# Optimization experiments

Hardware: AMD Instinct MI355X
Metric: run time of the kernel (lower is better)

## Reference

```python
import jax, jax.numpy as jnp
import numpy as np

# Mamba2 dims (from source: d_model=2048, d_state=64, d_conv=4, expand=2; defaults headdim=64, ngroups=1)
D_MODEL = 2048
D_STATE = 64
D_CONV = 4
EXPAND = 2
HEADDIM = 64
D_INNER = EXPAND * D_MODEL            # 4096
NHEADS = D_INNER // HEADDIM           # 64
NGROUPS = 1
CONV_DIM = D_INNER + 2 * NGROUPS * D_STATE   # 4224
D_IN_PROJ = 2 * D_INNER + 2 * NGROUPS * D_STATE + NHEADS  # 8384
N_CLASSES = 4
EPS = 1e-5


def setup_inputs() -> dict:
    key = jax.random.key(0)
    ks = jax.random.split(key, 10)
    b, l = 4, 2048
    x = jax.random.normal(ks[0], (b, l, D_MODEL), dtype=jnp.float32)
    in_proj_w = jax.random.normal(ks[1], (D_IN_PROJ, D_MODEL), dtype=jnp.float32) * 0.02
    conv_w = jax.random.normal(ks[2], (CONV_DIM, D_CONV), dtype=jnp.float32) * 0.2
    conv_b = jnp.zeros((CONV_DIM,), dtype=jnp.float32)
    # dt_bias s.t. softplus(dt_bias) in [0.001, 0.1]
    dt = jax.random.uniform(ks[3], (NHEADS,), minval=0.001, maxval=0.1)
    dt_bias = jnp.log(jnp.expm1(dt)).astype(jnp.float32)
    # A in [1, 16] per head
    A_log = jnp.log(jax.random.uniform(ks[4], (NHEADS,), minval=1.0, maxval=16.0)).astype(jnp.float32)
    D = jnp.ones((NHEADS,), dtype=jnp.float32)
    norm_w = jnp.ones((D_INNER,), dtype=jnp.float32)
    out_proj_w = jax.random.normal(ks[5], (D_MODEL, D_INNER), dtype=jnp.float32) * 0.02
    cls_w = jax.random.normal(ks[6], (N_CLASSES, D_MODEL), dtype=jnp.float32) * 0.02
    cls_b = jnp.zeros((N_CLASSES,), dtype=jnp.float32)
    return {"x": x, "in_proj_w": in_proj_w, "conv_w": conv_w, "conv_b": conv_b,
            "dt_bias": dt_bias, "A_log": A_log, "D": D, "norm_w": norm_w,
            "out_proj_w": out_proj_w, "cls_w": cls_w, "cls_b": cls_b}


def _mamba2_forward(x, in_proj_w, conv_w, conv_b, dt_bias, A_log, D, norm_w, out_proj_w):
    b, l, _ = x.shape
    zxbcdt = jnp.einsum('bld,ed->ble', x, in_proj_w)  # (b,l,8384)
    z = zxbcdt[..., :D_INNER]
    xBC = zxbcdt[..., D_INNER:D_INNER + CONV_DIM]
    dt_raw = zxbcdt[..., D_INNER + CONV_DIM:]         # (b,l,nheads)

    # causal depthwise conv1d (kernel D_CONV), then SiLU
    xp = jnp.pad(xBC, ((0, 0), (D_CONV - 1, 0), (0, 0)))
    conv_out = conv_b
    for k in range(D_CONV):
        conv_out = conv_out + xp[:, k:k + l, :] * conv_w[:, k]
    xBC = jax.nn.silu(conv_out)

    xh = xBC[..., :D_INNER].reshape(b, l, NHEADS, HEADDIM)
    Bm = xBC[..., D_INNER:D_INNER + D_STATE]          # (b,l,n) ngroups=1
    Cm = xBC[..., D_INNER + D_STATE:]                 # (b,l,n)

    dt = jax.nn.softplus(dt_raw + dt_bias)           # (b,l,h)
    dA = jnp.exp(dt * (-jnp.exp(A_log)))             # (b,l,h)
    dtx = dt[..., None] * xh                          # (b,l,h,p)

    xs = (dA.transpose(1, 0, 2), dtx.transpose(1, 0, 2, 3),
          Bm.transpose(1, 0, 2), Cm.transpose(1, 0, 2))

    def step(hst, inp):
        dA_t, dtx_t, B_t, C_t = inp
        # hst: (b,h,p,n)
        hst = hst * dA_t[:, :, None, None] + dtx_t[..., None] * B_t[:, None, None, :]
        y_t = jnp.einsum('bhpn,bn->bhp', hst, C_t)
        return hst, y_t

    h0 = jnp.zeros((b, NHEADS, HEADDIM, D_STATE), dtype=x.dtype)
    _, ys = jax.lax.scan(step, h0, xs)               # (l,b,h,p)
    y = ys.transpose(1, 0, 2, 3) + D[None, None, :, None] * xh
    y = y.reshape(b, l, D_INNER)

    # RMSNormGated (norm_before_gate=False): rmsnorm(y * silu(z)) * weight
    y = y * jax.nn.silu(z)
    y = y * jax.lax.rsqrt(jnp.mean(y * y, axis=-1, keepdims=True) + EPS) * norm_w
    return jnp.einsum('ble,de->bld', y, out_proj_w)   # (b,l,d_model)


def reference(x, in_proj_w, conv_w, conv_b, dt_bias, A_log, D, norm_w, out_proj_w, cls_w, cls_b):
    h = _mamba2_forward(x, in_proj_w, conv_w, conv_b, dt_bias, A_log, D, norm_w, out_proj_w)
    return jnp.einsum('bld,cd->blc', h, cls_w) + cls_b  # (b,l,4)
```

## Files before the change

kernel.cpp:

```cpp
#include <hip/hip_runtime.h>

#define BB 4
#define LL 2048
#define DMODEL 2048
#define DSTATE 64
#define DCONV 4
#define DINNER 4096
#define NHEADS 64
#define CONVDIM 4224
#define DINPROJ 8384
#define NPAD1   8448
#define MROWS 8192
#define DTROW0 8320
#define XBCCOLS 4288

typedef short bf16x8 __attribute__((ext_vector_type(8)));
typedef float f32x4  __attribute__((ext_vector_type(4)));
typedef __attribute__((address_space(1))) void as1_void;
typedef __attribute__((address_space(3))) void as3_void;

__device__ inline unsigned short f2bf(float f) {
  unsigned int u = __float_as_uint(f);
  u += 0x7FFF + ((u >> 16) & 1);
  return (unsigned short)(u >> 16);
}
__device__ inline float bf2f(unsigned short u) {
  return __uint_as_float(((unsigned int)u) << 16);
}

__global__ void f32_to_bf16_kernel(const float* __restrict__ in,
                                   unsigned short* __restrict__ out, long nquads) {
  long q = (long)blockIdx.x * 256 + threadIdx.x;
  if (q >= nquads) return;
  float4 v = ((const float4*)in)[q];
  ushort4 o;
  o.x = f2bf(v.x); o.y = f2bf(v.y); o.z = f2bf(v.z); o.w = f2bf(v.w);
  ((ushort4*)out)[q] = o;
}

__global__ void convert_w1_kernel(const float* __restrict__ w,
                                  unsigned short* __restrict__ out) {
  long q = (long)blockIdx.x * 256 + threadIdx.x;
  long row = q >> 9;
  ushort4 o; o.x = 0; o.y = 0; o.z = 0; o.w = 0;
  if (row < DINPROJ) {
    float4 v = ((const float4*)w)[q];
    o.x = f2bf(v.x); o.y = f2bf(v.y); o.z = f2bf(v.z); o.w = f2bf(v.w);
  }
  ((ushort4*)out)[q] = o;
}

template <bool BF16OUT, bool SPLIT>
__global__ __launch_bounds__(256) void gemm_mfma(
    const unsigned short* __restrict__ A,
    const unsigned short* __restrict__ B,
    void* __restrict__ Cv, void* __restrict__ Cv2,
    int M, int N, int K, int Nsplit, int ld2) {
  __shared__ __align__(16) char sA[128 * 128];
  __shared__ __align__(16) char sB[128 * 128];
  const int tid  = threadIdx.x;
  const int lane = tid & 63;
  const int wave = tid >> 6;
  const long m0 = (long)blockIdx.y * 128;
  const long n0 = (long)blockIdx.x * 128;
  const int wm = (wave >> 1) * 64;
  const int wn = (wave & 1) * 64;
  const int fr = lane & 15;
  const int kb = lane >> 4;
  const int xr = (fr & 7) << 4;
  const size_t strideA = (size_t)K * 2;

  f32x4 acc[4][4] = {};

  for (int k0 = 0; k0 < K; k0 += 64) {
    __syncthreads();
#pragma unroll
    for (int u = 0; u < 4; ++u) {
      const int idx  = u * 256 + tid;
      const int row  = idx >> 3;
      const int csrc = ((idx & 7) << 4) ^ ((row & 7) << 4);
      const char* ga = (const char*)A + (size_t)(m0 + row) * strideA + (size_t)k0 * 2 + csrc;
      const char* gb = (const char*)B + (size_t)(n0 + row) * strideA + (size_t)k0 * 2 + csrc;
      __builtin_amdgcn_global_load_lds((as1_void*)ga, (as3_void*)(sA + idx * 16), 16, 0, 0);
      __builtin_amdgcn_global_load_lds((as1_void*)gb, (as3_void*)(sB + idx * 16), 16, 0, 0);
    }
    __syncthreads();
#pragma unroll
    for (int kh = 0; kh < 2; ++kh) {
      bf16x8 af[4], bg[4];
      const int cread = (kh * 64 + kb * 16) ^ xr;
#pragma unroll
      for (int i = 0; i < 4; ++i) {
        const int ar = wm + i * 16 + fr;
        af[i] = *(const bf16x8*)(sA + ar * 128 + cread);
        const int br = wn + i * 16 + fr;
        bg[i] = *(const bf16x8*)(sB + br * 128 + cread);
      }
#pragma unroll
      for (int i = 0; i < 4; ++i)
#pragma unroll
        for (int j = 0; j < 4; ++j)
          acc[i][j] = __builtin_amdgcn_mfma_f32_16x16x32_bf16(af[i], bg[j], acc[i][j], 0, 0, 0);
    }
  }

#pragma unroll
  for (int i = 0; i < 4; ++i) {
    const long mbase = m0 + wm + i * 16 + kb * 4;
#pragma unroll
    for (int j = 0; j < 4; ++j) {
      const long n = n0 + wn + j * 16 + fr;
      if (n < N) {
#pragma unroll
        for (int r = 0; r < 4; ++r) {
          const long m = mbase + r;
          if (!SPLIT || n < Nsplit) {
            const long ld = SPLIT ? Nsplit : N;
            if (BF16OUT) ((unsigned short*)Cv)[m * ld + n] = f2bf(acc[i][j][r]);
            else         ((float*)Cv)[m * ld + n] = acc[i][j][r];
          } else {
            if (BF16OUT) ((unsigned short*)Cv2)[m * (long)ld2 + (n - Nsplit)] = f2bf(acc[i][j][r]);
            else         ((float*)Cv2)[m * (long)ld2 + (n - Nsplit)] = acc[i][j][r];
          }
        }
      }
    }
  }
}

__global__ void dt_kernel(const float* __restrict__ x,
                          const float* __restrict__ w,
                          const float* __restrict__ dt_bias,
                          const float* __restrict__ A_log,
                          float* __restrict__ dtv, float* __restrict__ dAv) {
  __shared__ float s_w[64][129];
  __shared__ float s_x[16][129];
  const int tid = threadIdx.x;
  const int row0 = blockIdx.x * 16;
  const int c = tid & 63;
  const int rg = tid >> 6;
  float acc[4] = {0.f, 0.f, 0.f, 0.f};
  for (int k0 = 0; k0 < DMODEL; k0 += 128) {
    __syncthreads();
#pragma unroll
    for (int u = 0; u < 32; ++u) {
      int idx = u * 256 + tid;
      int r = idx >> 7, kk = idx & 127;
      s_w[r][kk] = w[(size_t)(DTROW0 + r) * DMODEL + k0 + kk];
    }
#pragma unroll
    for (int u = 0; u < 8; ++u) {
      int idx = u * 256 + tid;
      int r = idx >> 7, kk = idx & 127;
      s_x[r][kk] = x[(size_t)(row0 + r) * DMODEL + k0 + kk];
    }
    __syncthreads();
    for (int kk = 0; kk < 128; ++kk) {
      float wv = s_w[c][kk];
#pragma unroll
      for (int j = 0; j < 4; ++j) acc[j] += s_x[rg * 4 + j][kk] * wv;
    }
  }
  const float a = expf(A_log[c]);
  const float bias = dt_bias[c];
#pragma unroll
  for (int j = 0; j < 4; ++j) {
    int row = row0 + rg * 4 + j;
    float v = acc[j] + bias;
    float dt = (v > 20.f) ? v : log1pf(expf(v));
    dtv[(size_t)row * 64 + c] = dt;
    dAv[(size_t)row * 64 + c] = expf(-dt * a);
  }
}

__global__ void conv_kernel(const unsigned short* __restrict__ xbc,
                            const float* __restrict__ conv_w,
                            const float* __restrict__ conv_b,
                            unsigned short* __restrict__ xh,
                            float* __restrict__ Bm,
                            float* __restrict__ Cm) {
  const int row = blockIdx.x;
  const int l = row & (LL - 1);
  for (int c = threadIdx.x; c < CONVDIM; c += 256) {
    float acc = conv_b[c];
#pragma unroll
    for (int k = 0; k < DCONV; ++k) {
      int ll = l - (DCONV - 1) + k;
      if (ll >= 0) {
        size_t rr = (size_t)row + (ll - l);
        acc += bf2f(xbc[rr * XBCCOLS + c]) * conv_w[c * DCONV + k];
      }
    }
    float s = acc / (1.f + expf(-acc));
    if (c < DINNER)               xh[(size_t)row * DINNER + c] = f2bf(s);
    else if (c < DINNER + DSTATE) Bm[(size_t)row * DSTATE + (c - DINNER)] = s;
    else                          Cm[(size_t)row * DSTATE + (c - DINNER - DSTATE)] = s;
  }
}

#define CT 16
#define CHUNK 128
#define NCHUNK 16

__global__ void scan_state_kernel(const unsigned short* __restrict__ xhp,
                                  const float* __restrict__ Bm,
                                  const float* __restrict__ dtv,
                                  const float* __restrict__ dAv,
                                  float* __restrict__ hend,
                                  float* __restrict__ chunkA) {
  __shared__ __align__(16) float s_x[CT][64];
  __shared__ __align__(16) float s_B[CT][64];
  __shared__ float s_dt[CT], s_dA[CT];
  const int chunk = blockIdx.x & (NCHUNK - 1);
  const int bh = blockIdx.x >> 4;
  const int head = bh & 63;
  const int b = bh >> 6;
  const int tid = threadIdx.x;
  const int p = tid >> 2, q = tid & 3, n0 = q * 16;
  float h[16];
#pragma unroll
  for (int i = 0; i < 16; ++i) h[i] = 0.f;
  float pA = 1.f;
  const int tbase = b * LL + chunk * CHUNK;

  for (int t0 = 0; t0 < CHUNK; t0 += CT) {
    __syncthreads();
#pragma unroll
    for (int u = 0; u < CT * 64 / 256; ++u) {
      int idx = u * 256 + tid;
      int tt = idx >> 6, cc = idx & 63;
      size_t r = (size_t)(tbase + t0 + tt);
      s_x[tt][cc] = bf2f(xhp[r * DINNER + head * 64 + cc]);
      s_B[tt][cc] = Bm[r * 64 + cc];
    }
    if (tid < CT) {
      size_t r = (size_t)(tbase + t0 + tid);
      s_dt[tid] = dtv[r * 64 + head];
      s_dA[tid] = dAv[r * 64 + head];
    }
    __syncthreads();
    for (int tt = 0; tt < CT; ++tt) {
      float dA = s_dA[tt];
      float dtx = s_dt[tt] * s_x[tt][p];
      pA *= dA;
      const float4* Bp = (const float4*)&s_B[tt][n0];
#pragma unroll
      for (int i = 0; i < 4; ++i) {
        float4 bv = Bp[i];
        h[4*i+0] = h[4*i+0] * dA + dtx * bv.x;
        h[4*i+1] = h[4*i+1] * dA + dtx * bv.y;
        h[4*i+2] = h[4*i+2] * dA + dtx * bv.z;
        h[4*i+3] = h[4*i+3] * dA + dtx * bv.w;
      }
    }
  }
  float* hp = hend + ((size_t)bh * NCHUNK + chunk) * 4096 + tid * 16;
#pragma unroll
  for (int i = 0; i < 4; ++i) {
    float4 v; v.x = h[4*i]; v.y = h[4*i+1]; v.z = h[4*i+2]; v.w = h[4*i+3];
    ((float4*)hp)[i] = v;
  }
  if (tid == 0) chunkA[bh * NCHUNK + chunk] = pA;
}

__global__ void scan_prop_kernel(float* __restrict__ hend,
                                 const float* __restrict__ chunkA) {
  const int bh = blockIdx.x;
  const int tid = threadIdx.x;
  float cr[16];
#pragma unroll
  for (int i = 0; i < 16; ++i) cr[i] = 0.f;
  for (int c = 0; c < NCHUNK; ++c) {
    float* hp = hend + ((size_t)bh * NCHUNK + c) * 4096 + tid * 16;
    const float a = chunkA[bh * NCHUNK + c];
    float e[16];
#pragma unroll
    for (int i = 0; i < 4; ++i) {
      float4 v = ((float4*)hp)[i];
      e[4*i] = v.x; e[4*i+1] = v.y; e[4*i+2] = v.z; e[4*i+3] = v.w;
    }
#pragma unroll
    for (int i = 0; i < 4; ++i) {
      float4 v; v.x = cr[4*i]; v.y = cr[4*i+1]; v.z = cr[4*i+2]; v.w = cr[4*i+3];
      ((float4*)hp)[i] = v;
    }
#pragma unroll
    for (int i = 0; i < 16; ++i) cr[i] = cr[i] * a + e[i];
  }
}

__global__ void scan_apply_kernel(const unsigned short* xhp,
                                  const float* __restrict__ Bm,
                                  const float* __restrict__ Cm,
                                  const float* __restrict__ dtv,
                                  const float* __restrict__ dAv,
                                  const float* __restrict__ Dv,
                                  const float* __restrict__ hstart,
                                  unsigned short* y) {
  __shared__ __align__(16) float s_x[CT][64];
  __shared__ __align__(16) float s_B[CT][64];
  __shared__ __align__(16) float s_C[CT][64];
  __shared__ __align__(16) float s_y[CT][64];
  __shared__ float s_dt[CT], s_dA[CT];
  const int chunk = blockIdx.x & (NCHUNK - 1);
  const int bh = blockIdx.x >> 4;
  const int head = bh & 63;
  const int b = bh >> 6;
  const int tid = threadIdx.x;
  const int p = tid >> 2, q = tid & 3, n0 = q * 16;
  const float Dh = Dv[head];
  const int tbase = b * LL + chunk * CHUNK;

  float h[16];
  {
    const float* hp = hstart + ((size_t)bh * NCHUNK + chunk) * 4096 + tid * 16;
#pragma unroll
    for (int i = 0; i < 4; ++i) {
      float4 v = ((const float4*)hp)[i];
      h[4*i] = v.x; h[4*i+1] = v.y; h[4*i+2] = v.z; h[4*i+3] = v.w;
    }
  }

  for (int t0 = 0; t0 < CHUNK; t0 += CT) {
    __syncthreads();
#pragma unroll
    for (int u = 0; u < CT * 64 / 256; ++u) {
      int idx = u * 256 + tid;
      int tt = idx >> 6, cc = idx & 63;
      size_t r = (size_t)(tbase + t0 + tt);
      s_x[tt][cc] = bf2f(xhp[r * DINNER + head * 64 + cc]);
      s_B[tt][cc] = Bm[r * 64 + cc];
      s_C[tt][cc] = Cm[r * 64 + cc];
    }
    if (tid < CT) {
      size_t r = (size_t)(tbase + t0 + tid);
      s_dt[tid] = dtv[r * 64 + head];
      s_dA[tid] = dAv[r * 64 + head];
    }
    __syncthreads();
    for (int tt = 0; tt < CT; ++tt) {
      float dA = s_dA[tt], dt = s_dt[tt];
      float xp = s_x[tt][p];
      float dtx = dt * xp;
      const float4* Bp = (const float4*)&s_B[tt][n0];
      const float4* Cp = (const float4*)&s_C[tt][n0];
      float ys = 0.f;
#pragma unroll
      for (int i = 0; i < 4; ++i) {
        float4 bv = Bp[i];
        float4 cv = Cp[i];
        h[4*i+0] = h[4*i+0] * dA + dtx * bv.x;  ys += h[4*i+0] * cv.x;
        h[4*i+1] = h[4*i+1] * dA + dtx * bv.y;  ys += h[4*i+1] * cv.y;
        h[4*i+2] = h[4*i+2] * dA + dtx * bv.z;  ys += h[4*i+2] * cv.z;
        h[4*i+3] = h[4*i+3] * dA + dtx * bv.w;  ys += h[4*i+3] * cv.w;
      }
      ys += __shfl_xor(ys, 1);
      ys += __shfl_xor(ys, 2);
      if (q == 0) s_y[tt][p] = ys + Dh * xp;
    }
    __syncthreads();
#pragma unroll
    for (int u = 0; u < CT * 64 / 256; ++u) {
      int idx = u * 256 + tid;
      int tt = idx >> 6, cc = idx & 63;
      size_t r = (size_t)(tbase + t0 + tt);
      y[r * DINNER + head * 64 + cc] = f2bf(s_y[tt][cc]);
    }
  }
}

__global__ void norm_kernel(const unsigned short* y,
                            const unsigned short* __restrict__ zbuf,
                            const float* __restrict__ norm_w,
                            unsigned short* ynb) {
  const int row = blockIdx.x;
  const int tid = threadIdx.x;
  float g[16];
  float ss = 0.f;
#pragma unroll
  for (int i = 0; i < 16; ++i) {
    int d = i * 256 + tid;
    float zv = bf2f(zbuf[(size_t)row * DINNER + d]);
    float gv = bf2f(y[(size_t)row * DINNER + d]) * (zv / (1.f + expf(-zv)));
    g[i] = gv;
    ss += gv * gv;
  }
#pragma unroll
  for (int off = 32; off >= 1; off >>= 1) ss += __shfl_xor(ss, off);
  __shared__ float sred[4];
  __shared__ float s_rs;
  if ((tid & 63) == 0) sred[tid >> 6] = ss;
  __syncthreads();
  if (tid == 0) {
    float tot = sred[0] + sred[1] + sred[2] + sred[3];
    s_rs = rsqrtf(tot / (float)DINNER + 1e-5f);
  }
  __syncthreads();
  float rs = s_rs;
#pragma unroll
  for (int i = 0; i < 16; ++i) {
    int d = i * 256 + tid;
    ynb[(size_t)row * DINNER + d] = f2bf(g[i] * rs * norm_w[d]);
  }
}

__global__ void cls_kernel(const float* __restrict__ h,
                           const float* __restrict__ cls_w,
                           const float* __restrict__ cls_b,
                           float* __restrict__ out) {
  const int row = blockIdx.x;
  const int tid = threadIdx.x;
  float a0 = 0, a1 = 0, a2 = 0, a3 = 0;
  for (int d = tid; d < DMODEL; d += 256) {
    float hv = h[(size_t)row * DMODEL + d];
    a0 += hv * cls_w[d];
    a1 += hv * cls_w[DMODEL + d];
    a2 += hv * cls_w[2 * DMODEL + d];
    a3 += hv * cls_w[3 * DMODEL + d];
  }
#pragma unroll
  for (int off = 32; off >= 1; off >>= 1) {
    a0 += __shfl_xor(a0, off); a1 += __shfl_xor(a1, off);
    a2 += __shfl_xor(a2, off); a3 += __shfl_xor(a3, off);
  }
  __shared__ float sred[4][4];
  if ((tid & 63) == 0) { int w = tid >> 6; sred[w][0] = a0; sred[w][1] = a1; sred[w][2] = a2; sred[w][3] = a3; }
  __syncthreads();
  if (tid < 4) {
    float s = sred[0][tid] + sred[1][tid] + sred[2][tid] + sred[3][tid] + cls_b[tid];
    out[(size_t)row * 4 + tid] = s;
  }
}

extern "C" void kernel_launch(void* const* d_in, const int* in_sizes, int n_in,
                              void* d_out, int out_size, void* d_ws, size_t ws_size,
                              hipStream_t stream) {
  const float* x          = (const float*)d_in[0];
  const float* in_proj_w  = (const float*)d_in[1];
  const float* conv_w     = (const float*)d_in[2];
  const float* conv_b     = (const float*)d_in[3];
  const float* dt_bias    = (const float*)d_in[4];
  const float* A_log      = (const float*)d_in[5];
  const float* Dv         = (const float*)d_in[6];
  const float* norm_w     = (const float*)d_in[7];
  const float* out_proj_w = (const float*)d_in[8];
  const float* cls_w      = (const float*)d_in[9];
  const float* cls_b      = (const float*)d_in[10];

  char* ws = (char*)d_ws;
  unsigned short* zbuf = (unsigned short*)(ws + 0);
  unsigned short* xbc  = (unsigned short*)(ws + 67108864);
  unsigned short* xh   = (unsigned short*)(ws + 137363456);
  float*          Bmp  = (float*)(ws + 204472320);
  float*          Cmp  = (float*)(ws + 206569472);
  float*          dtv  = (float*)(ws + 208666624);
  float*          dAv  = (float*)(ws + 210763776);
  unsigned short* ynb  = xh;
  float*          hbuf = (float*)zbuf;
  unsigned short* xbf = xh;
  unsigned short* w1b = (unsigned short*)((char*)xh + 33554432);
  float*          hend   = (float*)xbc;
  float*          chunkA = (float*)((char*)xbc + 67108864);
  unsigned short* w2b = (unsigned short*)xbc;

  f32_to_bf16_kernel<<<16384, 256, 0, stream>>>(x, xbf, 4194304);
  convert_w1_kernel<<<16896, 256, 0, stream>>>(in_proj_w, w1b);

  dt_kernel<<<512, 256, 0, stream>>>(x, in_proj_w, dt_bias, A_log, dtv, dAv);

  gemm_mfma<true, true><<<dim3(NPAD1 / 128, MROWS / 128), 256, 0, stream>>>(
      xbf, w1b, zbuf, xbc, MROWS, DINPROJ, DMODEL, DINNER, XBCCOLS);

  conv_kernel<<<MROWS, 256, 0, stream>>>(xbc, conv_w, conv_b, xh, Bmp, Cmp);

  scan_state_kernel<<<256 * NCHUNK, 256, 0, stream>>>(xh, Bmp, dtv, dAv, hend, chunkA);
  scan_prop_kernel<<<256, 256, 0, stream>>>(hend, chunkA);
  scan_apply_kernel<<<256 * NCHUNK, 256, 0, stream>>>(xh, Bmp, Cmp, dtv, dAv, Dv, hend, xh);

  norm_kernel<<<MROWS, 256, 0, stream>>>(xh, zbuf, norm_w, ynb);

  f32_to_bf16_kernel<<<8192, 256, 0, stream>>>(out_proj_w, w2b, 2097152);

  gemm_mfma<false, false><<<dim3(DMODEL / 128, MROWS / 128), 256, 0, stream>>>(
      ynb, w2b, hbuf, nullptr, MROWS, DMODEL, DINNER, DMODEL, 0);

  cls_kernel<<<MROWS, 256, 0, stream>>>(hbuf, cls_w, cls_b, (float*)d_out);
}
```

Before: 1.568 ms.

## Fold out_proj and classifier into one vector, vectorize conv and scan loads

The out_proj weight is premultiplied by the classifier weights into a 4x4096 matrix Wc. RMSNorm, gating and classification are then fused into a single per-row dot-product kernel. This removes the second large GEMM, its weight conversion and the separate cls pass. The change also vectorizes the conv kernel (8 channels per thread), the scan smem loads and stores, and adds XCD-aware block remapping to the GEMM. The algebraic fold is exact in math, but summation order and precision differ, since Wc is computed in fp32 and the activation is no longer rounded to bf16 before projection.

New measurement: 1.548 ms. Within noise of the previous version (-1.3%).

```diff
diff --git a/kernel.cpp b/kernel.cpp
--- a/kernel.cpp
+++ b/kernel.cpp
@@ -15,6 +15,7 @@
 #define XBCCOLS 4288
 
 typedef short bf16x8 __attribute__((ext_vector_type(8)));
+typedef short bf16x4 __attribute__((ext_vector_type(4)));
 typedef float f32x4  __attribute__((ext_vector_type(4)));
 typedef __attribute__((address_space(1))) void as1_void;
 typedef __attribute__((address_space(3))) void as3_void;
@@ -61,8 +62,14 @@
   const int tid  = threadIdx.x;
   const int lane = tid & 63;
   const int wave = tid >> 6;
-  const long m0 = (long)blockIdx.y * 128;
-  const long n0 = (long)blockIdx.x * 128;
+  const int nwg = gridDim.x * gridDim.y;
+  int lin = blockIdx.y * gridDim.x + blockIdx.x;
+  if ((nwg & 7) == 0) {
+    const int q = nwg >> 3;
+    lin = (lin & 7) * q + (lin >> 3);
+  }
+  const long m0 = (long)(lin / gridDim.x) * 128;
+  const long n0 = (long)(lin % gridDim.x) * 128;
   const int wm = (wave >> 1) * 64;
   const int wn = (wave & 1) * 64;
   const int fr = lane & 15;
@@ -181,20 +188,57 @@
                             float* __restrict__ Cm) {
   const int row = blockIdx.x;
   const int l = row & (LL - 1);
-  for (int c = threadIdx.x; c < CONVDIM; c += 256) {
-    float acc = conv_b[c];
+  const int tid = threadIdx.x;
+  for (int gsel = 0; gsel < 3; ++gsel) {
+    int g;
+    if (gsel == 0) g = tid;
+    else if (gsel == 1) g = tid + 256;
+    else { if (tid >= 16) break; g = 512 + tid; }
+    const int c0 = g * 8;
+    float cwa[8][4];
+#pragma unroll
+    for (int i = 0; i < 8; ++i) {
+      float4 cw = *(const float4*)&conv_w[(c0 + i) * 4];
+      cwa[i][0] = cw.x; cwa[i][1] = cw.y; cwa[i][2] = cw.z; cwa[i][3] = cw.w;
+    }
+    float acc[8];
+    {
+      float4 cb0 = *(const float4*)&conv_b[c0];
+      float4 cb1 = *(const float4*)&conv_b[c0 + 4];
+      acc[0] = cb0.x; acc[1] = cb0.y; acc[2] = cb0.z; acc[3] = cb0.w;
+      acc[4] = cb1.x; acc[5] = cb1.y; acc[6] = cb1.z; acc[7] = cb1.w;
+    }
 #pragma unroll
     for (int k = 0; k < DCONV; ++k) {
-      int ll = l - (DCONV - 1) + k;
+      const int ll = l - (DCONV - 1) + k;
       if (ll >= 0) {
-        size_t rr = (size_t)row + (ll - l);
-        acc += bf2f(xbc[rr * XBCCOLS + c]) * conv_w[c * DCONV + k];
+        const size_t rr = (size_t)(row - (DCONV - 1) + k);
+        bf16x8 v = *(const bf16x8*)&xbc[rr * XBCCOLS + c0];
+#pragma unroll
+        for (int i = 0; i < 8; ++i)
+          acc[i] += bf2f((unsigned short)v[i]) * cwa[i][k];
       }
     }
-    float s = acc / (1.f + expf(-acc));
-    if (c < DINNER)               xh[(size_t)row * DINNER + c] = f2bf(s);
-    else if (c < DINNER + DSTATE) Bm[(size_t)row * DSTATE + (c - DINNER)] = s;
-    else                          Cm[(size_t)row * DSTATE + (c - DINNER - DSTATE)] = s;
+    float s[8];
+#pragma unroll
+    for (int i = 0; i < 8; ++i) s[i] = acc[i] / (1.f + expf(-acc[i]));
+    if (g < 512) {
+      bf16x8 o;
+#pragma unroll
+      for (int i = 0; i < 8; ++i) o[i] = (short)f2bf(s[i]);
+      *(bf16x8*)&xh[(size_t)row * DINNER + c0] = o;
+    } else {
+      float4 o0, o1;
+      o0.x = s[0]; o0.y = s[1]; o0.z = s[2]; o0.w = s[3];
+      o1.x = s[4]; o1.y = s[5]; o1.z = s[6]; o1.w = s[7];
+      if (g < 520) {
+        float* p = &Bm[(size_t)row * DSTATE + (c0 - DINNER)];
+        ((float4*)p)[0] = o0; ((float4*)p)[1] = o1;
+      } else {
+        float* p = &Cm[(size_t)row * DSTATE + (c0 - DINNER - DSTATE)];
+        ((float4*)p)[0] = o0; ((float4*)p)[1] = o1;
+      }
+    }
   }
 }
 
@@ -217,6 +261,7 @@
   const int b = bh >> 6;
   const int tid = threadIdx.x;
   const int p = tid >> 2, q = tid & 3, n0 = q * 16;
+  const int stt = tid >> 4, scc = (tid & 15) * 4;
   float h[16];
 #pragma unroll
   for (int i = 0; i < 16; ++i) h[i] = 0.f;
@@ -225,13 +270,14 @@
 
   for (int t0 = 0; t0 < CHUNK; t0 += CT) {
     __syncthreads();
-#pragma unroll
-    for (int u = 0; u < CT * 64 / 256; ++u) {
-      int idx = u * 256 + tid;
-      int tt = idx >> 6, cc = idx & 63;
-      size_t r = (size_t)(tbase + t0 + tt);
-      s_x[tt][cc] = bf2f(xhp[r * DINNER + head * 64 + cc]);
-      s_B[tt][cc] = Bm[r * 64 + cc];
+    {
+      size_t r = (size_t)(tbase + t0 + stt);
+      bf16x4 xv = *(const bf16x4*)&xhp[r * DINNER + head * 64 + scc];
+      float4 xf;
+      xf.x = bf2f((unsigned short)xv[0]); xf.y = bf2f((unsigned short)xv[1]);
+      xf.z = bf2f((unsigned short)xv[2]); xf.w = bf2f((unsigned short)xv[3]);
+      *(float4*)&s_x[stt][scc] = xf;
+      *(float4*)&s_B[stt][scc] = *(const float4*)&Bm[r * 64 + scc];
     }
     if (tid < CT) {
       size_t r = (size_t)(tbase + t0 + tid);
@@ -308,6 +354,7 @@
   const int b = bh >> 6;
   const int tid = threadIdx.x;
   const int p = tid >> 2, q = tid & 3, n0 = q * 16;
+  const int stt = tid >> 4, scc = (tid & 15) * 4;
   const float Dh = Dv[head];
   const int tbase = b * LL + chunk * CHUNK;
 
@@ -323,14 +370,15 @@
 
   for (int t0 = 0; t0 < CHUNK; t0 += CT) {
     __syncthreads();
-#pragma unroll
-    for (int u = 0; u < CT * 64 / 256; ++u) {
-      int idx = u * 256 + tid;
-      int tt = idx >> 6, cc = idx & 63;
-      size_t r = (size_t)(tbase + t0 + tt);
-      s_x[tt][cc] = bf2f(xhp[r * DINNER + head * 64 + cc]);
-      s_B[tt][cc] = Bm[r * 64 + cc];
-      s_C[tt][cc] = Cm[r * 64 + cc];
+    {
+      size_t r = (size_t)(tbase + t0 + stt);
+      bf16x4 xv = *(const bf16x4*)&xhp[r * DINNER + head * 64 + scc];
+      float4 xf;
+      xf.x = bf2f((unsigned short)xv[0]); xf.y = bf2f((unsigned short)xv[1]);
+      xf.z = bf2f((unsigned short)xv[2]); xf.w = bf2f((unsigned short)xv[3]);
+      *(float4*)&s_x[stt][scc] = xf;
+      *(float4*)&s_B[stt][scc] = *(const float4*)&Bm[r * 64 + scc];
+      *(float4*)&s_C[stt][scc] = *(const float4*)&Cm[r * 64 + scc];
     }
     if (tid < CT) {
       size_t r = (size_t)(tbase + t0 + tid);
@@ -359,31 +407,59 @@
       if (q == 0) s_y[tt][p] = ys + Dh * xp;
     }
     __syncthreads();
-#pragma unroll
-    for (int u = 0; u < CT * 64 / 256; ++u) {
-      int idx = u * 256 + tid;
-      int tt = idx >> 6, cc = idx & 63;
-      size_t r = (size_t)(tbase + t0 + tt);
-      y[r * DINNER + head * 64 + cc] = f2bf(s_y[tt][cc]);
-    }
-  }
-}
-
-__global__ void norm_kernel(const unsigned short* y,
-                            const unsigned short* __restrict__ zbuf,
-                            const float* __restrict__ norm_w,
-                            unsigned short* ynb) {
+    {
+      size_t r = (size_t)(tbase + t0 + stt);
+      float4 yv = *(const float4*)&s_y[stt][scc];
+      bf16x4 o;
+      o[0] = (short)f2bf(yv.x); o[1] = (short)f2bf(yv.y);
+      o[2] = (short)f2bf(yv.z); o[3] = (short)f2bf(yv.w);
+      *(bf16x4*)&y[r * DINNER + head * 64 + scc] = o;
+    }
+  }
+}
+
+__global__ void wc_kernel(const float* __restrict__ W,
+                          const float* __restrict__ C,
+                          float* __restrict__ Wc) {
+  const int e = blockIdx.x * 256 + threadIdx.x;
+  float a0 = 0, a1 = 0, a2 = 0, a3 = 0;
+  for (int d = 0; d < DMODEL; ++d) {
+    float wv = W[(size_t)d * DINNER + e];
+    a0 += C[d] * wv;
+    a1 += C[DMODEL + d] * wv;
+    a2 += C[2 * DMODEL + d] * wv;
+    a3 += C[3 * DMODEL + d] * wv;
+  }
+  Wc[e] = a0; Wc[DINNER + e] = a1; Wc[2 * DINNER + e] = a2; Wc[3 * DINNER + e] = a3;
+}
+
+__global__ void normcls_kernel(const unsigned short* __restrict__ y,
+                               const unsigned short* __restrict__ z,
+                               const float* __restrict__ norm_w,
+                               const float* __restrict__ Wc,
+                               const float* __restrict__ cls_b,
+                               float* __restrict__ out) {
   const int row = blockIdx.x;
   const int tid = threadIdx.x;
+  const int d0 = tid * 16;
+  const size_t base = (size_t)row * DINNER + d0;
+  bf16x8 yv0 = *(const bf16x8*)&y[base];
+  bf16x8 yv1 = *(const bf16x8*)&y[base + 8];
+  bf16x8 zv0 = *(const bf16x8*)&z[base];
+  bf16x8 zv1 = *(const bf16x8*)&z[base + 8];
   float g[16];
   float ss = 0.f;
 #pragma unroll
-  for (int i = 0; i < 16; ++i) {
-    int d = i * 256 + tid;
-    float zv = bf2f(zbuf[(size_t)row * DINNER + d]);
-    float gv = bf2f(y[(size_t)row * DINNER + d]) * (zv / (1.f + expf(-zv)));
-    g[i] = gv;
-    ss += gv * gv;
+  for (int i = 0; i < 8; ++i) {
+    float zz = bf2f((unsigned short)zv0[i]);
+    float gv = bf2f((unsigned short)yv0[i]) * (zz / (1.f + expf(-zz)));
+    g[i] = gv; ss += gv * gv;
+  }
+#pragma unroll
+  for (int i = 0; i < 8; ++i) {
+    float zz = bf2f((unsigned short)zv1[i]);
+    float gv = bf2f((unsigned short)yv1[i]) * (zz / (1.f + expf(-zz)));
+    g[8 + i] = gv; ss += gv * gv;
   }
 #pragma unroll
   for (int off = 32; off >= 1; off >>= 1) ss += __shfl_xor(ss, off);
@@ -391,45 +467,41 @@
   __shared__ float s_rs;
   if ((tid & 63) == 0) sred[tid >> 6] = ss;
   __syncthreads();
-  if (tid == 0) {
-    float tot = sred[0] + sred[1] + sred[2] + sred[3];
-    s_rs = rsqrtf(tot / (float)DINNER + 1e-5f);
-  }
+  if (tid == 0)
+    s_rs = rsqrtf((sred[0] + sred[1] + sred[2] + sred[3]) / (float)DINNER + 1e-5f);
   __syncthreads();
-  float rs = s_rs;
-#pragma unroll
-  for (int i = 0; i < 16; ++i) {
-    int d = i * 256 + tid;
-    ynb[(size_t)row * DINNER + d] = f2bf(g[i] * rs * norm_w[d]);
-  }
-}
-
-__global__ void cls_kernel(const float* __restrict__ h,
-                           const float* __restrict__ cls_w,
-                           const float* __restrict__ cls_b,
-                           float* __restrict__ out) {
-  const int row = blockIdx.x;
-  const int tid = threadIdx.x;
-  float a0 = 0, a1 = 0, a2 = 0, a3 = 0;
-  for (int d = tid; d < DMODEL; d += 256) {
-    float hv = h[(size_t)row * DMODEL + d];
-    a0 += hv * cls_w[d];
-    a1 += hv * cls_w[DMODEL + d];
-    a2 += hv * cls_w[2 * DMODEL + d];
-    a3 += hv * cls_w[3 * DMODEL + d];
+  const float rs = s_rs;
+  float gn[16];
+#pragma unroll
+  for (int j = 0; j < 4; ++j) {
+    float4 nw = *(const float4*)&norm_w[d0 + j * 4];
+    gn[j*4+0] = g[j*4+0] * rs * nw.x;
+    gn[j*4+1] = g[j*4+1] * rs * nw.y;
+    gn[j*4+2] = g[j*4+2] * rs * nw.z;
+    gn[j*4+3] = g[j*4+3] * rs * nw.w;
+  }
+  float a[4] = {0.f, 0.f, 0.f, 0.f};
+#pragma unroll
+  for (int c = 0; c < 4; ++c) {
+#pragma unroll
+    for (int j = 0; j < 4; ++j) {
+      float4 w4 = *(const float4*)&Wc[c * DINNER + d0 + j * 4];
+      a[c] += gn[j*4+0]*w4.x + gn[j*4+1]*w4.y + gn[j*4+2]*w4.z + gn[j*4+3]*w4.w;
+    }
   }
 #pragma unroll
   for (int off = 32; off >= 1; off >>= 1) {
-    a0 += __shfl_xor(a0, off); a1 += __shfl_xor(a1, off);
-    a2 += __shfl_xor(a2, off); a3 += __shfl_xor(a3, off);
-  }
-  __shared__ float sred[4][4];
-  if ((tid & 63) == 0) { int w = tid >> 6; sred[w][0] = a0; sred[w][1] = a1; sred[w][2] = a2; sred[w][3] = a3; }
+#pragma unroll
+    for (int c = 0; c < 4; ++c) a[c] += __shfl_xor(a[c], off);
+  }
+  __shared__ float s4[4][4];
+  if ((tid & 63) == 0) {
+    int w = tid >> 6;
+    s4[w][0] = a[0]; s4[w][1] = a[1]; s4[w][2] = a[2]; s4[w][3] = a[3];
+  }
   __syncthreads();
-  if (tid < 4) {
-    float s = sred[0][tid] + sred[1][tid] + sred[2][tid] + sred[3][tid] + cls_b[tid];
-    out[(size_t)row * 4 + tid] = s;
-  }
+  if (tid < 4)
+    out[(size_t)row * 4 + tid] = s4[0][tid] + s4[1][tid] + s4[2][tid] + s4[3][tid] + cls_b[tid];
 }
 
 extern "C" void kernel_launch(void* const* d_in, const int* in_sizes, int n_in,
@@ -455,13 +527,11 @@
   float*          Cmp  = (float*)(ws + 206569472);
   float*          dtv  = (float*)(ws + 208666624);
   float*          dAv  = (float*)(ws + 210763776);
-  unsigned short* ynb  = xh;
-  float*          hbuf = (float*)zbuf;
   unsigned short* xbf = xh;
   unsigned short* w1b = (unsigned short*)((char*)xh + 33554432);
   float*          hend   = (float*)xbc;
-  float*          chunkA = (float*)((char*)xbc + 67108864);
-  unsigned short* w2b = (unsigned short*)xbc;
+  float*          chunkA = (float*)(ws + 134217728);
+  float*          Wcp    = (float*)(ws + 134234112);
 
   f32_to_bf16_kernel<<<16384, 256, 0, stream>>>(x, xbf, 4194304);
   convert_w1_kernel<<<16896, 256, 0, stream>>>(in_proj_w, w1b);
@@ -472,17 +542,12 @@
       xbf, w1b, zbuf, xbc, MROWS, DINPROJ, DMODEL, DINNER, XBCCOLS);
 
   conv_kernel<<<MROWS, 256, 0, stream>>>(xbc, conv_w, conv_b, xh, Bmp, Cmp);
+
+  wc_kernel<<<16, 256, 0, stream>>>(out_proj_w, cls_w, Wcp);
 
   scan_state_kernel<<<256 * NCHUNK, 256, 0, stream>>>(xh, Bmp, dtv, dAv, hend, chunkA);
   scan_prop_kernel<<<256, 256, 0, stream>>>(hend, chunkA);
   scan_apply_kernel<<<256 * NCHUNK, 256, 0, stream>>>(xh, Bmp, Cmp, dtv, dAv, Dv, hend, xh);
 
-  norm_kernel<<<MROWS, 256, 0, stream>>>(xh, zbuf, norm_w, ynb);
-
-  f32_to_bf16_kernel<<<8192, 256, 0, stream>>>(out_proj_w, w2b, 2097152);
-
-  gemm_mfma<false, false><<<dim3(DMODEL / 128, MROWS / 128), 256, 0, stream>>>(
-      ynb, w2b, hbuf, nullptr, MROWS, DMODEL, DINNER, DMODEL, 0);
-
-  cls_kernel<<<MROWS, 256, 0, stream>>>(hbuf, cls_w, cls_b, (float*)d_out);
-}
+  normcls_kernel<<<MROWS, 256, 0, stream>>>(xh, zbuf, norm_w, Wcp, cls_b, (float*)d_out);
+}
```
